# Optimization experiments

Measured on AMD Instinct MI355X. Metric: run time of the kernel, lower is better.

## Reference

```python
import jax, jax.numpy as jnp
import numpy as np

TAU = 3.0      # time horizon (init arg tau)
FIX = 0.2      # correction gain (init arg fix)


def setup_inputs() -> dict:
    key = jax.random.key(0)
    k1, k2, k3, k4, k5 = jax.random.split(key, 5)
    B, N, K = 256, 1024, 32
    p_cur = jax.random.normal(k1, (B, N, 2), dtype=jnp.float32) * 10.0   # positions (meters)
    v_cur = jax.random.normal(k2, (B, N, 2), dtype=jnp.float32)          # previous velocities
    v_desire = jax.random.normal(k3, (B, N, 2), dtype=jnp.float32)       # desired velocities
    near_ped_idx = jax.random.randint(k4, (B, N, K), 0, N, dtype=jnp.int32)
    neigh_ped_mask = jax.random.randint(k5, (B, N, K), 0, 2).astype(jnp.float32)
    return {
        "p_cur": p_cur,
        "v_cur": v_cur,
        "v_desire": v_desire,
        "near_ped_idx": near_ped_idx,
        "neigh_ped_mask": neigh_ped_mask,
        "collision_threshold": 1,
    }


def reference(p_cur, v_cur, v_desire, near_ped_idx, neigh_ped_mask, collision_threshold):
    # Gather neighbor positions/velocities: (B,N,K,2). vmap over batch avoids
    # materializing the (B,N,N,2) expanded tensor the torch code logically builds.
    gather = jax.vmap(lambda arr, idx: arr[idx])
    neighbors_pos = gather(p_cur, near_ped_idx)
    neighbors_vel = gather(v_cur, near_ped_idx)

    mask = neigh_ped_mask[..., None]                      # (B,N,K,1)
    neighbors_pos = neighbors_pos * mask
    neighbors_vel = neighbors_vel * mask

    rel_pos = p_cur[:, :, None, :] - neighbors_pos        # (B,N,K,2)
    rel_vel = v_desire[:, :, None, :] - neighbors_vel     # (B,N,K,2)

    dot_pos_vel = jnp.sum(rel_pos * rel_vel, axis=-1)     # (B,N,K)
    dot_vel_vel = jnp.sum(rel_vel * rel_vel, axis=-1) + 1e-6
    t_min = dot_pos_vel / (dot_vel_vel + 1e-6)
    t_min = jnp.where(jnp.isnan(t_min), TAU, t_min)
    t_clamp = jnp.clip(t_min, 0.0, TAU)

    min_dist = jnp.linalg.norm(rel_pos + t_clamp[..., None] * rel_vel, axis=-1)
    min_dist = jnp.where(jnp.isnan(min_dist), 1e6, min_dist)

    collision_mask = (min_dist < collision_threshold) & (neigh_ped_mask != 0)

    # 90-degree rotated rel_pos as collision normal
    normal = jnp.stack([-rel_pos[..., 1], rel_pos[..., 0]], axis=-1)   # (B,N,K,2)
    denom = jnp.linalg.norm(normal, axis=-1, keepdims=True)
    normal = jnp.where(collision_mask[..., None], normal / (denom + 1e-6), 0.0)

    correction = jnp.sum(normal, axis=2)                  # (B,N,2)
    correction = jnp.nan_to_num(correction, nan=0.0)
    v_next = v_desire + correction * FIX
    return v_next
```

## Files before the change

kernel.cpp:

```cpp
#include <hip/hip_runtime.h>

#define TAU 3.0f
#define FIX 0.2f
#define NPED 1024
#define PEDS_PER_BLOCK 256
#define BLOCK 512
#define GROUPS (BLOCK / 8)
#define PASSES (PEDS_PER_BLOCK / GROUPS)

__global__ __launch_bounds__(BLOCK) void rvo_kernel(
    const float* __restrict__ p_cur,
    const float* __restrict__ v_cur,
    const float* __restrict__ v_desire,
    const int*   __restrict__ near_idx,
    const float* __restrict__ mask_arr,
    const int*   __restrict__ cth,
    float*       __restrict__ out,
    int N)
{
    __shared__ float4 table[NPED];

    const int tid    = threadIdx.x;
    const int bpb    = N / PEDS_PER_BLOCK;
    const int batch  = blockIdx.x / bpb;
    const int pbase  = (blockIdx.x % bpb) * PEDS_PER_BLOCK;

    const float2* pb2 = (const float2*)(p_cur) + (size_t)batch * N;
    const float2* vb2 = (const float2*)(v_cur) + (size_t)batch * N;
    #pragma unroll
    for (int n = tid; n < NPED; n += BLOCK) {
        float2 pp = pb2[n];
        float2 vv = vb2[n];
        table[n] = make_float4(pp.x, pp.y, vv.x, vv.y);
    }
    __syncthreads();

    const float thr2 = (float)cth[0] * (float)cth[0];

    const int sub  = tid & 7;
    const int pgrp = tid >> 3;
    const size_t base = (size_t)batch * N + pbase + pgrp;

    const int4*   idx4  = (const int4*)near_idx;
    const float4* msk4  = (const float4*)mask_arr;
    const float2* vd2   = (const float2*)v_desire;

    int4   i4 = idx4[base * 8 + sub];
    float4 m4 = msk4[base * 8 + sub];

    #pragma unroll
    for (int pass = 0; pass < PASSES; ++pass) {
        const int4   ci = i4;
        const float4 cm = m4;
        if (pass + 1 < PASSES) {
            const size_t npair = base + (size_t)(pass + 1) * GROUPS;
            i4 = idx4[npair * 8 + sub];
            m4 = msk4[npair * 8 + sub];
        }

        const int ped  = pbase + pass * GROUPS + pgrp;
        const size_t pair = base + (size_t)pass * GROUPS;

        const float4 self = table[ped];
        const float2 vd   = vd2[pair];
        const float px = self.x, py = self.y;
        const float vdx = vd.x, vdy = vd.y;

        const int   idxs[4] = {ci.x, ci.y, ci.z, ci.w};
        const float ms[4]   = {cm.x, cm.y, cm.z, cm.w};

        float nx = 0.0f, ny = 0.0f;
        #pragma unroll
        for (int j = 0; j < 4; ++j) {
            const float4 nb = table[idxs[j]];
            const float m = ms[j];
            const float rpx = fmaf(-m, nb.x, px);
            const float rpy = fmaf(-m, nb.y, py);
            const float rvx = fmaf(-m, nb.z, vdx);
            const float rvy = fmaf(-m, nb.w, vdy);

            const float dpv = fmaf(rpx, rvx, rpy * rvy);
            const float dvv = fmaf(rvx, rvx, fmaf(rvy, rvy, 2e-6f));
            float t = dpv * __builtin_amdgcn_rcpf(dvv);
            t = fminf(fmaxf(t, 0.0f), TAU);

            const float cx = fmaf(t, rvx, rpx);
            const float cy = fmaf(t, rvy, rpy);
            const float md2 = fmaf(cx, cx, cy * cy);

            const float s = fmaf(rpx, rpx, rpy * rpy);
            const float sel0 = (s > 0.0f) ? __builtin_amdgcn_rsqf(s) : 0.0f;
            const float w    = (md2 < thr2) ? m : 0.0f;
            const float sel  = sel0 * w;
            nx = fmaf(-rpy, sel, nx);
            ny = fmaf( rpx, sel, ny);
        }

        #pragma unroll
        for (int d = 4; d > 0; d >>= 1) {
            nx += __shfl_down(nx, d, 8);
            ny += __shfl_down(ny, d, 8);
        }

        if (sub == 0) {
            ((float2*)out)[pair] = make_float2(fmaf(nx, FIX, vdx),
                                               fmaf(ny, FIX, vdy));
        }
    }
}

extern "C" void kernel_launch(void* const* d_in, const int* in_sizes, int n_in,
                              void* d_out, int out_size, void* d_ws, size_t ws_size,
                              hipStream_t stream) {
    const float* p_cur    = (const float*)d_in[0];
    const float* v_cur    = (const float*)d_in[1];
    const float* v_desire = (const float*)d_in[2];
    const int*   near_idx = (const int*)d_in[3];
    const float* mask_arr = (const float*)d_in[4];
    const int*   cth      = (const int*)d_in[5];
    float*       out      = (float*)d_out;

    const int N  = NPED;
    const int BN = in_sizes[0] / 2;
    dim3 block(BLOCK);
    dim3 grid(BN / PEDS_PER_BLOCK);
    rvo_kernel<<<grid, block, 0, stream>>>(p_cur, v_cur, v_desire, near_idx,
                                           mask_arr, cth, out, N);
}
```

Measured before the change: 112.0 us.

## Split LDS neighbor table into float2 arrays and drop manual index prefetch

Replaces the interleaved float4 shared-memory table with separate float2 position and velocity arrays, so each random neighbor lookup becomes two 8-byte LDS reads instead of one 16-byte read. It also removes the software prefetch of the next pass's index and mask vectors and loads them inline, leaving latency hiding to the compiler and the hardware. This may change LDS bank-conflict behaviour on the random gathers, but it doubles the number of LDS instructions and could expose global load latency.

```diff
diff --git a/kernel.cpp b/kernel.cpp
--- a/kernel.cpp
+++ b/kernel.cpp
@@ -18,7 +18,8 @@
     float*       __restrict__ out,
     int N)
 {
-    __shared__ float4 table[NPED];
+    __shared__ float2 tpos[NPED];
+    __shared__ float2 tvel[NPED];
 
     const int tid    = threadIdx.x;
     const int bpb    = N / PEDS_PER_BLOCK;
@@ -29,9 +30,8 @@
     const float2* vb2 = (const float2*)(v_cur) + (size_t)batch * N;
     #pragma unroll
     for (int n = tid; n < NPED; n += BLOCK) {
-        float2 pp = pb2[n];
-        float2 vv = vb2[n];
-        table[n] = make_float4(pp.x, pp.y, vv.x, vv.y);
+        tpos[n] = pb2[n];
+        tvel[n] = vb2[n];
     }
     __syncthreads();
 
@@ -39,45 +39,32 @@
 
     const int sub  = tid & 7;
     const int pgrp = tid >> 3;
-    const size_t base = (size_t)batch * N + pbase + pgrp;
-
-    const int4*   idx4  = (const int4*)near_idx;
-    const float4* msk4  = (const float4*)mask_arr;
-    const float2* vd2   = (const float2*)v_desire;
-
-    int4   i4 = idx4[base * 8 + sub];
-    float4 m4 = msk4[base * 8 + sub];
 
     #pragma unroll
     for (int pass = 0; pass < PASSES; ++pass) {
-        const int4   ci = i4;
-        const float4 cm = m4;
-        if (pass + 1 < PASSES) {
-            const size_t npair = base + (size_t)(pass + 1) * GROUPS;
-            i4 = idx4[npair * 8 + sub];
-            m4 = msk4[npair * 8 + sub];
-        }
+        const int ped  = pbase + pass * GROUPS + pgrp;
+        const size_t pair = (size_t)batch * N + ped;
 
-        const int ped  = pbase + pass * GROUPS + pgrp;
-        const size_t pair = base + (size_t)pass * GROUPS;
-
-        const float4 self = table[ped];
-        const float2 vd   = vd2[pair];
+        const float2 self = tpos[ped];
+        const float2 vd   = ((const float2*)v_desire)[pair];
         const float px = self.x, py = self.y;
         const float vdx = vd.x, vdy = vd.y;
 
-        const int   idxs[4] = {ci.x, ci.y, ci.z, ci.w};
-        const float ms[4]   = {cm.x, cm.y, cm.z, cm.w};
+        const int4   i4 = ((const int4*)near_idx)[pair * 8 + sub];
+        const float4 m4 = ((const float4*)mask_arr)[pair * 8 + sub];
+        const int   idxs[4] = {i4.x, i4.y, i4.z, i4.w};
+        const float ms[4]   = {m4.x, m4.y, m4.z, m4.w};
 
         float nx = 0.0f, ny = 0.0f;
         #pragma unroll
         for (int j = 0; j < 4; ++j) {
-            const float4 nb = table[idxs[j]];
+            const float2 nbp = tpos[idxs[j]];
+            const float2 nbv = tvel[idxs[j]];
             const float m = ms[j];
-            const float rpx = fmaf(-m, nb.x, px);
-            const float rpy = fmaf(-m, nb.y, py);
-            const float rvx = fmaf(-m, nb.z, vdx);
-            const float rvy = fmaf(-m, nb.w, vdy);
+            const float rpx = fmaf(-m, nbp.x, px);
+            const float rpy = fmaf(-m, nbp.y, py);
+            const float rvx = fmaf(-m, nbv.x, vdx);
+            const float rvy = fmaf(-m, nbv.y, vdy);
 
             const float dpv = fmaf(rpx, rvx, rpy * rvy);
             const float dvv = fmaf(rvx, rvx, fmaf(rvy, rvy, 2e-6f));
```

Result: faster. 106.3 us (-5.2%).
